# Kernel tuning notes

Measured on AMD Instinct MI355X. Metric: run time of the kernel, lower is better.

The kernel has to match this reference:

```python
import jax, jax.numpy as jnp
import numpy as np

N, D, K = 524288, 256, 64
ALPHA = 1.0


def setup_inputs() -> dict:
    key = jax.random.key(0)
    k1, k2 = jax.random.split(key)
    inputs = jax.random.normal(k1, (N, D), dtype=jnp.float32)
    clusters = jax.random.normal(k2, (K, D), dtype=jnp.float32)  # glorot-init stand-in
    return {"inputs": inputs, "clusters": clusters}


def reference(inputs, clusters):
    # Squared euclidean distance ||x - c||^2 via GEMM expansion: same math as
    # sum((x[:,None,:] - c[None,:,:])**2, -1) without the (N,K,D) intermediate.
    x2 = jnp.sum(inputs * inputs, axis=1, keepdims=True)          # (N,1)
    c2 = jnp.sum(clusters * clusters, axis=1)                     # (K,)
    d2 = x2 + c2 - 2.0 * (inputs @ clusters.T)                    # (N,K)
    d2 = jnp.maximum(d2, 0.0)                                     # numeric guard
    q = 1.0 / (1.0 + d2 / ALPHA)                                  # Student-t kernel
    q = q ** ((ALPHA + 1.0) / 2.0)
    return q / jnp.sum(q, axis=1, keepdims=True)                  # row-normalize
```

## Files before the change

### kernel.cpp

```cpp
#include <hip/hip_runtime.h>
#include <hip/hip_bf16.h>

#define NPTS 524288
#define DIM 256
#define KC 64

typedef __attribute__((ext_vector_type(8))) short bf16x8;
typedef __attribute__((ext_vector_type(4))) float f32x4;

typedef __attribute__((address_space(1))) const unsigned int GUI;
typedef __attribute__((address_space(3))) unsigned int LUI;

static __device__ __forceinline__ void gload16(const void* g, void* l) {
  __builtin_amdgcn_global_load_lds((GUI*)g, (LUI*)l, 16, 0, 0);
}

static __device__ __forceinline__ ushort f32_to_bf16_rne(float f) {
  unsigned int b = __builtin_bit_cast(unsigned int, f);
  b += 0x7FFFu + ((b >> 16) & 1u);
  return (ushort)(b >> 16);
}

__global__ void prep_clusters(const float* __restrict__ C,
                              char* __restrict__ cb,
                              float* __restrict__ c2) {
  const int w = threadIdx.x >> 6;
  const int lane = threadIdx.x & 63;
  const int k = blockIdx.x * 8 + w * 2 + (lane >> 5);
  const int m = lane & 31;
  const float* src = C + k * DIM + m * 8;
  float4 u0 = ((const float4*)src)[0];
  float4 u1 = ((const float4*)src)[1];
  float vv[8] = {u0.x, u0.y, u0.z, u0.w, u1.x, u1.y, u1.z, u1.w};
  float s = 0.f;
  bf16x8 h;
#pragma unroll
  for (int j = 0; j < 8; ++j) {
    s = fmaf(vv[j], vv[j], s);
    h[j] = (short)f32_to_bf16_rne(vv[j]);
  }
  s += __shfl_xor(s, 1);
  s += __shfl_xor(s, 2);
  s += __shfl_xor(s, 4);
  s += __shfl_xor(s, 8);
  s += __shfl_xor(s, 16);
  const int slot = 16 * (k & 3) + (k >> 2);
  const int off = slot * 512 + ((m ^ (slot & 7)) << 4);
  *(bf16x8*)(cb + off) = h;
  if (m == 0) c2[k] = s;
}

__global__ __launch_bounds__(256, 2)
void cluster_q(const float* __restrict__ A, const char* __restrict__ cb,
               const float* __restrict__ c2, float* __restrict__ out) {
  __shared__ char lds[65536];
  const int tid = threadIdx.x;
  const int lane = tid & 63;
  const int w = tid >> 6;
  const int l15 = lane & 15;
  const int g = lane >> 4;
  const long brow = (long)blockIdx.x * 64;

  {
    const char* src = cb + w * 8192 + lane * 16;
    char* dst = lds + w * 8192;
#pragma unroll
    for (int i = 0; i < 8; ++i)
      gload16(src + i * 1024, dst + i * 1024);
  }

  const char* Arow0 = (const char*)A + (brow + w * 16) * (DIM * 4);

#define STAGE_A(ck, half)                                                    \
  do {                                                                       \
    char* dbase = lds + 32768 + w * 8192 + (half) * 4096;                    \
    _Pragma("unroll") for (int c = 0; c < 4; ++c) {                          \
      int o = c * 1024 + lane * 16;                                          \
      int row = o >> 8;                                                      \
      int kb = ((((o >> 4) & 15) ^ (row & 7)) << 4);                         \
      gload16(Arow0 + row * 1024 + (ck) * 256 + kb, dbase + c * 1024);       \
    }                                                                        \
  } while (0)

  STAGE_A(0, 0);
  STAGE_A(1, 1);
  __syncthreads();

  f32x4 acc[4];
#pragma unroll
  for (int t = 0; t < 4; ++t) acc[t] = (f32x4){0.f, 0.f, 0.f, 0.f};
  float x2l = 0.f;

#define KSTEP(ck, s2)                                                        \
  do {                                                                       \
    const char* abuf = lds + 32768 + w * 8192 + ((ck) & 1) * 4096;           \
    int ga = (s2) * 8 + g * 2;                                               \
    int a0 = l15 * 256 + ((ga ^ (l15 & 7)) << 4);                            \
    float4 u0 = *(const float4*)(abuf + a0);                                 \
    float4 u1 = *(const float4*)(abuf + (a0 ^ 16));                          \
    float vv[8] = {u0.x, u0.y, u0.z, u0.w, u1.x, u1.y, u1.z, u1.w};          \
    bf16x8 af;                                                               \
    _Pragma("unroll") for (int j = 0; j < 8; ++j) {                          \
      x2l = fmaf(vv[j], vv[j], x2l);                                         \
      af[j] = (short)f32_to_bf16_rne(vv[j]);                                 \
    }                                                                        \
    int ks = (ck) * 2 + (s2);                                                \
    _Pragma("unroll") for (int t = 0; t < 4; ++t) {                          \
      int slot = l15 + 16 * t;                                               \
      bf16x8 bf = *(const bf16x8*)(lds + slot * 512 +                        \
                                   (((ks * 4 + g) ^ (slot & 7)) << 4));      \
      acc[t] = __builtin_amdgcn_mfma_f32_16x16x32_bf16(af, bf, acc[t], 0, 0, 0); \
    }                                                                        \
  } while (0)

  asm volatile("s_waitcnt vmcnt(4)" ::: "memory");
  KSTEP(0, 0); KSTEP(0, 1);
  STAGE_A(2, 0);
  asm volatile("s_waitcnt vmcnt(4)" ::: "memory");
  KSTEP(1, 0); KSTEP(1, 1);
  STAGE_A(3, 1);
  asm volatile("s_waitcnt vmcnt(4)" ::: "memory");
  KSTEP(2, 0); KSTEP(2, 1);
  asm volatile("s_waitcnt vmcnt(0)" ::: "memory");
  KSTEP(3, 0); KSTEP(3, 1);

  x2l += __shfl_xor(x2l, 16);
  x2l += __shfl_xor(x2l, 32);
  float x2r[4];
#pragma unroll
  for (int r = 0; r < 4; ++r) x2r[r] = __shfl(x2l, g * 4 + r);

  float4 c2v = *(const float4*)(c2 + 4 * l15);
  float c2a[4] = {c2v.x, c2v.y, c2v.z, c2v.w};

  float qv[4][4];
  float rsum[4] = {0.f, 0.f, 0.f, 0.f};
#pragma unroll
  for (int t = 0; t < 4; ++t) {
#pragma unroll
    for (int r = 0; r < 4; ++r) {
      float d2 = fmaxf(x2r[r] + c2a[t] - 2.0f * acc[t][r], 0.f);
      float qq = __builtin_amdgcn_rcpf(1.0f + d2);
      qv[t][r] = qq;
      rsum[r] += qq;
    }
  }
#pragma unroll
  for (int r = 0; r < 4; ++r) {
    rsum[r] += __shfl_xor(rsum[r], 1);
    rsum[r] += __shfl_xor(rsum[r], 2);
    rsum[r] += __shfl_xor(rsum[r], 4);
    rsum[r] += __shfl_xor(rsum[r], 8);
    float inv = __builtin_amdgcn_rcpf(rsum[r]);
    long orow = brow + w * 16 + g * 4 + r;
    float4 o4 = {qv[0][r] * inv, qv[1][r] * inv, qv[2][r] * inv, qv[3][r] * inv};
    *(float4*)(out + orow * 64 + 4 * l15) = o4;
  }
#undef STAGE_A
#undef KSTEP
}

extern "C" void kernel_launch(void* const* d_in, const int* in_sizes, int n_in,
                              void* d_out, int out_size, void* d_ws, size_t ws_size,
                              hipStream_t stream) {
  const float* inputs = (const float*)d_in[0];
  const float* clusters = (const float*)d_in[1];
  float* out = (float*)d_out;

  char* cb = (char*)d_ws;
  float* c2 = (float*)((char*)d_ws + 32768);

  prep_clusters<<<8, 256, 0, stream>>>(clusters, cb, c2);
  cluster_q<<<NPTS / 64, 256, 0, stream>>>(inputs, cb, c2, out);
}
```

Baseline: 133.9 us.

## Process four 64-row tiles per block with a continuous double-buffered A pipeline

Each block now handles 256 input rows in four 64-row passes instead of one, so the grid shrinks fourfold. The bf16 cluster tile staged into LDS is loaded once per block and reused across all four passes, which cuts repeated 32 KB cluster loads from L2. The A-chunk prefetch now runs across pass boundaries, so the next pass's loads overlap the current epilogue. The cost is fewer blocks and a longer hand-tuned wait-count schedule that has to be kept consistent.

Result: slower. 140.9 us (+5.2%).

```diff
diff --git a/kernel.cpp b/kernel.cpp
--- a/kernel.cpp
+++ b/kernel.cpp
@@ -59,7 +59,7 @@
   const int w = tid >> 6;
   const int l15 = lane & 15;
   const int g = lane >> 4;
-  const long brow = (long)blockIdx.x * 64;
+  const long brow = (long)blockIdx.x * 256;
 
   {
     const char* src = cb + w * 8192 + lane * 16;
@@ -69,31 +69,23 @@
       gload16(src + i * 1024, dst + i * 1024);
   }
 
-  const char* Arow0 = (const char*)A + (brow + w * 16) * (DIM * 4);
-
-#define STAGE_A(ck, half)                                                    \
-  do {                                                                       \
-    char* dbase = lds + 32768 + w * 8192 + (half) * 4096;                    \
-    _Pragma("unroll") for (int c = 0; c < 4; ++c) {                          \
-      int o = c * 1024 + lane * 16;                                          \
+  const char* Abase = (const char*)A + (brow + w * 16) * 1024;
+
+#define STAGE(ci)                                                            \
+  do {                                                                       \
+    char* dbase = lds + 32768 + w * 8192 + ((ci) & 1) * 4096;                \
+    const char* sbase = Abase + ((ci) >> 2) * 65536 + ((ci) & 3) * 256;      \
+    _Pragma("unroll") for (int c4 = 0; c4 < 4; ++c4) {                       \
+      int o = c4 * 1024 + lane * 16;                                         \
       int row = o >> 8;                                                      \
-      int kb = ((((o >> 4) & 15) ^ (row & 7)) << 4);                         \
-      gload16(Arow0 + row * 1024 + (ck) * 256 + kb, dbase + c * 1024);       \
-    }                                                                        \
-  } while (0)
-
-  STAGE_A(0, 0);
-  STAGE_A(1, 1);
-  __syncthreads();
-
-  f32x4 acc[4];
-#pragma unroll
-  for (int t = 0; t < 4; ++t) acc[t] = (f32x4){0.f, 0.f, 0.f, 0.f};
-  float x2l = 0.f;
-
-#define KSTEP(ck, s2)                                                        \
-  do {                                                                       \
-    const char* abuf = lds + 32768 + w * 8192 + ((ck) & 1) * 4096;           \
+      int swz = ((((o >> 4) & 15) ^ (row & 7)) << 4);                        \
+      gload16(sbase + row * 1024 + swz, dbase + c4 * 1024);                  \
+    }                                                                        \
+  } while (0)
+
+#define KSTEP(c, s2)                                                         \
+  do {                                                                       \
+    const char* abuf = lds + 32768 + w * 8192 + ((c) & 1) * 4096;            \
     int ga = (s2) * 8 + g * 2;                                               \
     int a0 = l15 * 256 + ((ga ^ (l15 & 7)) << 4);                            \
     float4 u0 = *(const float4*)(abuf + a0);                                 \
@@ -104,7 +96,7 @@
       x2l = fmaf(vv[j], vv[j], x2l);                                         \
       af[j] = (short)f32_to_bf16_rne(vv[j]);                                 \
     }                                                                        \
-    int ks = (ck) * 2 + (s2);                                                \
+    int ks = ((c) & 3) * 2 + (s2);                                           \
     _Pragma("unroll") for (int t = 0; t < 4; ++t) {                          \
       int slot = l15 + 16 * t;                                               \
       bf16x8 bf = *(const bf16x8*)(lds + slot * 512 +                        \
@@ -113,51 +105,96 @@
     }                                                                        \
   } while (0)
 
-  asm volatile("s_waitcnt vmcnt(4)" ::: "memory");
-  KSTEP(0, 0); KSTEP(0, 1);
-  STAGE_A(2, 0);
-  asm volatile("s_waitcnt vmcnt(4)" ::: "memory");
-  KSTEP(1, 0); KSTEP(1, 1);
-  STAGE_A(3, 1);
-  asm volatile("s_waitcnt vmcnt(4)" ::: "memory");
-  KSTEP(2, 0); KSTEP(2, 1);
-  asm volatile("s_waitcnt vmcnt(0)" ::: "memory");
-  KSTEP(3, 0); KSTEP(3, 1);
-
-  x2l += __shfl_xor(x2l, 16);
-  x2l += __shfl_xor(x2l, 32);
-  float x2r[4];
-#pragma unroll
-  for (int r = 0; r < 4; ++r) x2r[r] = __shfl(x2l, g * 4 + r);
-
-  float4 c2v = *(const float4*)(c2 + 4 * l15);
-  float c2a[4] = {c2v.x, c2v.y, c2v.z, c2v.w};
-
-  float qv[4][4];
-  float rsum[4] = {0.f, 0.f, 0.f, 0.f};
-#pragma unroll
-  for (int t = 0; t < 4; ++t) {
-#pragma unroll
-    for (int r = 0; r < 4; ++r) {
-      float d2 = fmaxf(x2r[r] + c2a[t] - 2.0f * acc[t][r], 0.f);
-      float qq = __builtin_amdgcn_rcpf(1.0f + d2);
-      qv[t][r] = qq;
-      rsum[r] += qq;
-    }
-  }
-#pragma unroll
-  for (int r = 0; r < 4; ++r) {
-    rsum[r] += __shfl_xor(rsum[r], 1);
-    rsum[r] += __shfl_xor(rsum[r], 2);
-    rsum[r] += __shfl_xor(rsum[r], 4);
-    rsum[r] += __shfl_xor(rsum[r], 8);
-    float inv = __builtin_amdgcn_rcpf(rsum[r]);
-    long orow = brow + w * 16 + g * 4 + r;
-    float4 o4 = {qv[0][r] * inv, qv[1][r] * inv, qv[2][r] * inv, qv[3][r] * inv};
-    *(float4*)(out + orow * 64 + 4 * l15) = o4;
-  }
-#undef STAGE_A
+#define CHUNK(c)                                                             \
+  do {                                                                       \
+    KSTEP(c, 0);                                                             \
+    KSTEP(c, 1);                                                             \
+    if ((c) + 2 < 16) STAGE((c) + 2);                                        \
+  } while (0)
+
+#define V0 asm volatile("s_waitcnt vmcnt(0)" ::: "memory")
+#define V4 asm volatile("s_waitcnt vmcnt(4)" ::: "memory")
+#define V8 asm volatile("s_waitcnt vmcnt(8)" ::: "memory")
+
+#define INIT                                                                 \
+  do {                                                                       \
+    _Pragma("unroll") for (int t = 0; t < 4; ++t)                            \
+        acc[t] = (f32x4){0.f, 0.f, 0.f, 0.f};                                \
+    x2l = 0.f;                                                               \
+  } while (0)
+
+#define EPI(p)                                                               \
+  do {                                                                       \
+    x2l += __shfl_xor(x2l, 16);                                              \
+    x2l += __shfl_xor(x2l, 32);                                              \
+    float x2r[4];                                                            \
+    _Pragma("unroll") for (int r = 0; r < 4; ++r)                            \
+        x2r[r] = __shfl(x2l, g * 4 + r);                                     \
+    float4 c2v = *(const float4*)(c2 + 4 * l15);                             \
+    float c2a[4] = {c2v.x, c2v.y, c2v.z, c2v.w};                             \
+    float qv[4][4];                                                          \
+    float rsum[4] = {0.f, 0.f, 0.f, 0.f};                                    \
+    _Pragma("unroll") for (int t = 0; t < 4; ++t) {                          \
+      _Pragma("unroll") for (int r = 0; r < 4; ++r) {                        \
+        float d2 = fmaxf(x2r[r] + c2a[t] - 2.0f * acc[t][r], 0.f);           \
+        float qq = __builtin_amdgcn_rcpf(1.0f + d2);                         \
+        qv[t][r] = qq;                                                       \
+        rsum[r] += qq;                                                       \
+      }                                                                      \
+    }                                                                        \
+    _Pragma("unroll") for (int r = 0; r < 4; ++r) {                          \
+      rsum[r] += __shfl_xor(rsum[r], 1);                                     \
+      rsum[r] += __shfl_xor(rsum[r], 2);                                     \
+      rsum[r] += __shfl_xor(rsum[r], 4);                                     \
+      rsum[r] += __shfl_xor(rsum[r], 8);                                     \
+      float inv = __builtin_amdgcn_rcpf(rsum[r]);                            \
+      long orow = brow + (p) * 64 + w * 16 + g * 4 + r;                      \
+      float4 o4 = {qv[0][r] * inv, qv[1][r] * inv, qv[2][r] * inv,           \
+                   qv[3][r] * inv};                                          \
+      *(float4*)(out + orow * 64 + 4 * l15) = o4;                            \
+    }                                                                        \
+  } while (0)
+
+  f32x4 acc[4];
+  float x2l;
+
+  STAGE(0);
+  STAGE(1);
+  __syncthreads();
+
+  INIT;
+        CHUNK(0);
+        CHUNK(1);
+   V4;  CHUNK(2);
+   V4;  CHUNK(3);
+  EPI(0);
+  INIT;
+   V8;  CHUNK(4);
+   V8;  CHUNK(5);
+   V4;  CHUNK(6);
+   V4;  CHUNK(7);
+  EPI(1);
+  INIT;
+   V8;  CHUNK(8);
+   V8;  CHUNK(9);
+  V4;  CHUNK(10);
+  V4;  CHUNK(11);
+  EPI(2);
+  INIT;
+  V8;  CHUNK(12);
+  V8;  CHUNK(13);
+  V4;  CHUNK(14);
+  V0;  CHUNK(15);
+  EPI(3);
+
+#undef STAGE
 #undef KSTEP
+#undef CHUNK
+#undef V0
+#undef V4
+#undef V8
+#undef INIT
+#undef EPI
 }
 
 extern "C" void kernel_launch(void* const* d_in, const int* in_sizes, int n_in,
@@ -171,5 +208,5 @@
   float* c2 = (float*)((char*)d_ws + 32768);
 
   prep_clusters<<<8, 256, 0, stream>>>(clusters, cb, c2);
-  cluster_q<<<NPTS / 64, 256, 0, stream>>>(inputs, cb, c2, out);
-}
+  cluster_q<<<NPTS / 256, 256, 0, stream>>>(inputs, cb, c2, out);
+}
```

## Load A directly into registers with a rolling prefetch instead of LDS staging

Applied to the files above, without the earlier changes.

The input-row tiles no longer go through LDS via global_load_lds. Each lane now loads its own float4 pairs from global memory straight into registers, with a three-buffer rotation that prefetches two k-steps ahead. LDS drops to 32 KB, holding only the clusters, and launch bounds rise to 4 blocks per CU for more occupancy. The bf16 conversion now uses the library intrinsic, and the per-lane 32-byte strided global loads may coalesce less well than the old staged copies.

Result: faster. 131.2 us (-2.0%).

```diff
diff --git a/kernel.cpp b/kernel.cpp
--- a/kernel.cpp
+++ b/kernel.cpp
@@ -19,6 +19,10 @@
   unsigned int b = __builtin_bit_cast(unsigned int, f);
   b += 0x7FFFu + ((b >> 16) & 1u);
   return (ushort)(b >> 16);
+}
+
+static __device__ __forceinline__ short f2bf(float f) {
+  return __builtin_bit_cast(short, __float2bfloat16(f));
 }
 
 __global__ void prep_clusters(const float* __restrict__ C,
@@ -50,16 +54,23 @@
   if (m == 0) c2[k] = s;
 }
 
-__global__ __launch_bounds__(256, 2)
+__global__ __launch_bounds__(256, 4)
 void cluster_q(const float* __restrict__ A, const char* __restrict__ cb,
                const float* __restrict__ c2, float* __restrict__ out) {
-  __shared__ char lds[65536];
+  __shared__ char lds[32768];
   const int tid = threadIdx.x;
   const int lane = tid & 63;
   const int w = tid >> 6;
   const int l15 = lane & 15;
   const int g = lane >> 4;
   const long brow = (long)blockIdx.x * 64;
+
+  const char* Ap = (const char*)A + (brow + w * 16 + l15) * 1024 + g * 32;
+
+  float4 b0a = *(const float4*)(Ap + 0 * 128);
+  float4 b0b = *(const float4*)(Ap + 0 * 128 + 16);
+  float4 b1a = *(const float4*)(Ap + 1 * 128);
+  float4 b1b = *(const float4*)(Ap + 1 * 128 + 16);
 
   {
     const char* src = cb + w * 8192 + lane * 16;
@@ -68,61 +79,43 @@
     for (int i = 0; i < 8; ++i)
       gload16(src + i * 1024, dst + i * 1024);
   }
-
-  const char* Arow0 = (const char*)A + (brow + w * 16) * (DIM * 4);
-
-#define STAGE_A(ck, half)                                                    \
-  do {                                                                       \
-    char* dbase = lds + 32768 + w * 8192 + (half) * 4096;                    \
-    _Pragma("unroll") for (int c = 0; c < 4; ++c) {                          \
-      int o = c * 1024 + lane * 16;                                          \
-      int row = o >> 8;                                                      \
-      int kb = ((((o >> 4) & 15) ^ (row & 7)) << 4);                         \
-      gload16(Arow0 + row * 1024 + (ck) * 256 + kb, dbase + c * 1024);       \
-    }                                                                        \
-  } while (0)
-
-  STAGE_A(0, 0);
-  STAGE_A(1, 1);
   __syncthreads();
 
   f32x4 acc[4];
 #pragma unroll
   for (int t = 0; t < 4; ++t) acc[t] = (f32x4){0.f, 0.f, 0.f, 0.f};
   float x2l = 0.f;
+  float4 b2a, b2b;
 
-#define KSTEP(ck, s2)                                                        \
+#define KSTEP(ks, CA, CB, PA, PB)                                            \
   do {                                                                       \
-    const char* abuf = lds + 32768 + w * 8192 + ((ck) & 1) * 4096;           \
-    int ga = (s2) * 8 + g * 2;                                               \
-    int a0 = l15 * 256 + ((ga ^ (l15 & 7)) << 4);                            \
-    float4 u0 = *(const float4*)(abuf + a0);                                 \
-    float4 u1 = *(const float4*)(abuf + (a0 ^ 16));                          \
-    float vv[8] = {u0.x, u0.y, u0.z, u0.w, u1.x, u1.y, u1.z, u1.w};          \
+    float vv[8] = {CA.x, CA.y, CA.z, CA.w, CB.x, CB.y, CB.z, CB.w};          \
+    if ((ks) + 2 < 8) {                                                      \
+      PA = *(const float4*)(Ap + ((ks) + 2) * 128);                          \
+      PB = *(const float4*)(Ap + ((ks) + 2) * 128 + 16);                     \
+    }                                                                        \
     bf16x8 af;                                                               \
     _Pragma("unroll") for (int j = 0; j < 8; ++j) {                          \
       x2l = fmaf(vv[j], vv[j], x2l);                                         \
-      af[j] = (short)f32_to_bf16_rne(vv[j]);                                 \
+      af[j] = f2bf(vv[j]);                                                   \
     }                                                                        \
-    int ks = (ck) * 2 + (s2);                                                \
     _Pragma("unroll") for (int t = 0; t < 4; ++t) {                          \
       int slot = l15 + 16 * t;                                               \
       bf16x8 bf = *(const bf16x8*)(lds + slot * 512 +                        \
-                                   (((ks * 4 + g) ^ (slot & 7)) << 4));      \
+                                   ((((ks) * 4 + g) ^ (slot & 7)) << 4));    \
       acc[t] = __builtin_amdgcn_mfma_f32_16x16x32_bf16(af, bf, acc[t], 0, 0, 0); \
     }                                                                        \
   } while (0)
 
-  asm volatile("s_waitcnt vmcnt(4)" ::: "memory");
-  KSTEP(0, 0); KSTEP(0, 1);
-  STAGE_A(2, 0);
-  asm volatile("s_waitcnt vmcnt(4)" ::: "memory");
-  KSTEP(1, 0); KSTEP(1, 1);
-  STAGE_A(3, 1);
-  asm volatile("s_waitcnt vmcnt(4)" ::: "memory");
-  KSTEP(2, 0); KSTEP(2, 1);
-  asm volatile("s_waitcnt vmcnt(0)" ::: "memory");
-  KSTEP(3, 0); KSTEP(3, 1);
+  KSTEP(0, b0a, b0b, b2a, b2b);
+  KSTEP(1, b1a, b1b, b0a, b0b);
+  KSTEP(2, b2a, b2b, b1a, b1b);
+  KSTEP(3, b0a, b0b, b2a, b2b);
+  KSTEP(4, b1a, b1b, b0a, b0b);
+  KSTEP(5, b2a, b2b, b1a, b1b);
+  KSTEP(6, b0a, b0b, b0a, b0b);
+  KSTEP(7, b1a, b1b, b0a, b0b);
+#undef KSTEP
 
   x2l += __shfl_xor(x2l, 16);
   x2l += __shfl_xor(x2l, 32);
@@ -156,8 +149,6 @@
     float4 o4 = {qv[0][r] * inv, qv[1][r] * inv, qv[2][r] * inv, qv[3][r] * inv};
     *(float4*)(out + orow * 64 + 4 * l15) = o4;
   }
-#undef STAGE_A
-#undef KSTEP
 }
 
 extern "C" void kernel_launch(void* const* d_in, const int* in_sizes, int n_in,
```
